# Kernel tuning notes

Hardware: AMD Instinct MI355X
Metric: run time of the kernel (lower is better)

## Reference

```python
import jax, jax.numpy as jnp
import numpy as np

B, T, M, C, H = 256, 512, 16, 16, 768  # batch, time, n_media, ctrl_dim, gru hidden


def setup_inputs() -> dict:
    key = jax.random.key(0)
    ks = jax.random.split(key, 16)
    def nrm(k, shape, s=0.05):
        return jax.random.normal(k, shape, jnp.float32) * s
    A = jnp.triu(jnp.ones((M, M), jnp.float32), 1)  # strict-upper DAG prior
    return dict(
        Xm=jax.random.uniform(ks[0], (B, T, M), jnp.float32),
        Xc=jax.random.normal(ks[1], (B, T, C), jnp.float32),
        R=jax.random.randint(ks[2], (B,), 0, 2),
        A=A,
        edge_w1=nrm(ks[3], (M, 2 * M)), edge_b1=jnp.zeros((M,), jnp.float32),
        edge_w2=nrm(ks[4], (M, M)), edge_b2=jnp.zeros((M,), jnp.float32),
        node_w=nrm(ks[5], (M, 2 * M)), node_b=jnp.zeros((M,), jnp.float32),
        W_ih=nrm(ks[6], (3 * H, M + C)), W_hh=nrm(ks[7], (3 * H, H)),
        b_ih=jnp.zeros((3 * H,), jnp.float32), b_hh=jnp.zeros((3 * H,), jnp.float32),
        wraw_w=nrm(ks[8], (M, H), 0.01), wraw_b=jnp.zeros((M,), jnp.float32),
        alpha=jnp.full((M,), 0.5, jnp.float32),
        hill_a=jax.random.uniform(ks[9], (M,), jnp.float32) * 0.8 + 0.6,
        hill_g=jax.random.uniform(ks[10], (M,), jnp.float32) * 0.3 + 0.1,
        ctrl_w=nrm(ks[11], (H, C)), ctrl_b=jnp.zeros((H,), jnp.float32),
        reg_emb=nrm(ks[12], (2, H)),
        bias=jnp.zeros((1,), jnp.float32),
        h0=jnp.zeros((1, 1, H), jnp.float32),
    )


def reference(Xm, Xc, R, A, edge_w1, edge_b1, edge_w2, edge_b2, node_w, node_b,
              W_ih, W_hh, b_ih, b_hh, wraw_w, wraw_b, alpha, hill_a, hill_g,
              ctrl_w, ctrl_b, reg_emb, bias, h0):
    Bq = Xm.shape[0]
    # --- CausalEncoder, fully batched over (B, T) ---
    send = Xm @ A.T                      # [B,T,M]
    recv = Xm @ A
    He = jax.nn.relu(jnp.concatenate([send, recv], -1) @ edge_w1.T + edge_b1)
    He = jax.nn.relu(He @ edge_w2.T + edge_b2)
    Z = jax.nn.relu(jnp.concatenate([Xm, He], -1) @ node_w.T + node_b)  # [B,T,M]
    # --- adstock: linear recurrence along time via scan ---
    a = jnp.clip(alpha, 0.0, 1.0)
    xt = jnp.swapaxes(Xm, 0, 1)          # [T,B,M]
    def ad_step(prev, x):
        cur = x + a * prev
        return cur, cur
    _, rest = jax.lax.scan(ad_step, xt[0], xt[1:])
    ads = jnp.swapaxes(jnp.concatenate([xt[:1], rest], 0), 0, 1)  # [B,T,M]
    cmax = jnp.maximum(jnp.max(ads, axis=1, keepdims=True), 1e-6)
    x_n = ads / cmax
    # --- hill saturation ---
    ha = jnp.clip(hill_a, 0.1, 3.0)
    hg = jnp.clip(hill_g, 0.1, 2.0)
    num = jnp.maximum(x_n, 0.0) ** ha
    hill = num / (num + hg ** ha + 1e-8)
    # --- GRU (PyTorch gate order r,z,n) via scan ---
    gru_in = jnp.concatenate([hill + Z, Xc], -1)       # [B,T,M+C]
    git = jnp.swapaxes(gru_in, 0, 1)                   # [T,B,M+C]
    h_init = jnp.broadcast_to(h0[0, 0], (Bq, h0.shape[-1]))
    def gru_step(h, x):
        gi = x @ W_ih.T + b_ih
        gh = h @ W_hh.T + b_hh
        ir, iz, inn = jnp.split(gi, 3, axis=-1)
        hr, hz, hn = jnp.split(gh, 3, axis=-1)
        r = jax.nn.sigmoid(ir + hr)
        z = jax.nn.sigmoid(iz + hz)
        n = jnp.tanh(inn + r * hn)
        h_new = (1.0 - z) * n + z * h
        return h_new, h_new
    _, hs = jax.lax.scan(gru_step, h_init, git)
    h_seq = jnp.swapaxes(hs, 0, 1)                     # [B,T,H]
    # --- coefficients + output heads ---
    w_pos = jax.nn.softplus(h_seq @ wraw_w.T + wraw_b)  # [B,T,M]
    w0 = 0.5 * jax.lax.stop_gradient(w_pos[:, 1]) + 0.5 * w_pos[:, 0]
    w_pos = w_pos.at[:, 0].set(w0)
    contrib = hill * w_pos
    media_term = contrib.sum(-1)                        # [B,T]
    ctrl_term = jax.nn.relu(Xc @ ctrl_w.T + ctrl_b).sum(-1) * 0.3
    reg_term = reg_emb[0].sum() * 0.3                   # original indexes with zeros
    y_scaled = media_term + ctrl_term + reg_term + bias[0]
    return y_scaled, w_pos, contrib
```

## Files before the change

### kernel.cpp

```cpp
#include <hip/hip_runtime.h>

typedef __bf16 bf16;
typedef bf16 bf16x8 __attribute__((ext_vector_type(8)));
typedef bf16 bf16x4 __attribute__((ext_vector_type(4)));
typedef float f32x4 __attribute__((ext_vector_type(4)));

#define MFMA16(a,b,c) __builtin_amdgcn_mfma_f32_16x16x32_bf16((a),(b),(c),0,0,0)

#define B_N 256
#define T_N 512
#define H_N 768
#define WROW 776
#define WIHROW 40

__device__ float    g_ctrl[B_N * T_N];
__device__ bf16     g_hbuf[2 * B_N * H_N];
__device__ unsigned g_flag[256 * 32];
__device__ unsigned g_members[8 * 32];
__device__ unsigned g_roster[8];
__device__ unsigned g_sync;

__device__ __forceinline__ float sigmoidf_(float x){ return 1.f/(1.f+__expf(-x)); }
__device__ __forceinline__ float tanhf_(float x){
  float e = __expf(-2.f*fabsf(x));
  float t = (1.f-e)/(1.f+e);
  return copysignf(t, x);
}
__device__ __forceinline__ float softplusf_(float x){
  return x > 20.f ? x : log1pf(__expf(x));
}

__global__ void k_zero() {
  const int tid = threadIdx.x;
  for (int i = tid; i < 256*32; i += 256) g_flag[i] = 0u;
  if (tid < 256) g_members[tid & 255] = 0u;
  if (tid < 8)   g_roster[tid] = 0u;
  if (tid == 0)  g_sync = 0u;
}

__global__ __launch_bounds__(256) void k_encode(
    const float* __restrict__ Xm, const float* __restrict__ Xc,
    const float* __restrict__ Aw,
    const float* __restrict__ ew1, const float* __restrict__ eb1,
    const float* __restrict__ ew2, const float* __restrict__ eb2,
    const float* __restrict__ nw,  const float* __restrict__ nb,
    const float* __restrict__ cw,  const float* __restrict__ cb,
    float* __restrict__ Zout)
{
  __shared__ float sA[16][16], sE1[16][32], sE2[16][16], sNW[16][32];
  __shared__ float sEB1[16], sEB2[16], sNB[16];
  __shared__ float sCW[768][16];
  __shared__ float sCB[768];
  const int tid = threadIdx.x;
  for (int i = tid; i < 256; i += 256) sA[i>>4][i&15] = Aw[i];
  for (int i = tid; i < 512; i += 256) sE1[i>>5][i&31] = ew1[i];
  for (int i = tid; i < 256; i += 256) sE2[i>>4][i&15] = ew2[i];
  for (int i = tid; i < 512; i += 256) sNW[i>>5][i&31] = nw[i];
  if (tid < 16) { sEB1[tid]=eb1[tid]; sEB2[tid]=eb2[tid]; sNB[tid]=nb[tid]; }
  for (int i = tid; i < 768*16; i += 256) sCW[i>>4][i&15] = cw[i];
  for (int i = tid; i < 768; i += 256) sCB[i] = cb[i];
  __syncthreads();
  const int idx = blockIdx.x*256 + tid;
  const float* xmp = Xm + (size_t)idx*16;
  const float* xcp = Xc + (size_t)idx*16;
  float xm[16], xc[16];
  #pragma unroll
  for (int j=0;j<4;j++){
    *(f32x4*)&xm[j*4] = *(const f32x4*)(xmp + j*4);
    *(f32x4*)&xc[j*4] = *(const f32x4*)(xcp + j*4);
  }
  float snd[16], rcv[16];
  #pragma unroll
  for (int i=0;i<16;i++){
    float s=0.f, r=0.f;
    #pragma unroll
    for (int j=0;j<16;j++){ s += xm[j]*sA[i][j]; r += xm[j]*sA[j][i]; }
    snd[i]=s; rcv[i]=r;
  }
  float he[16];
  #pragma unroll
  for (int i=0;i<16;i++){
    float a = sEB1[i];
    #pragma unroll
    for (int k=0;k<16;k++) a += snd[k]*sE1[i][k];
    #pragma unroll
    for (int k=0;k<16;k++) a += rcv[k]*sE1[i][16+k];
    he[i] = fmaxf(a, 0.f);
  }
  float he2[16];
  #pragma unroll
  for (int i=0;i<16;i++){
    float a = sEB2[i];
    #pragma unroll
    for (int k=0;k<16;k++) a += he[k]*sE2[i][k];
    he2[i] = fmaxf(a, 0.f);
  }
  float* zp = Zout + (size_t)idx*16;
  #pragma unroll
  for (int m=0;m<16;m++){
    float a = sNB[m];
    #pragma unroll
    for (int k=0;k<16;k++) a += xm[k]*sNW[m][k];
    #pragma unroll
    for (int k=0;k<16;k++) a += he2[k]*sNW[m][16+k];
    zp[m] = fmaxf(a, 0.f);
  }
  float cs = 0.f;
  for (int i=0;i<768;i++){
    float a = sCB[i];
    #pragma unroll
    for (int k=0;k<16;k++) a += xc[k]*sCW[i][k];
    cs += fmaxf(a, 0.f);
  }
  g_ctrl[idx] = cs * 0.3f;
}

__global__ __launch_bounds__(64) void k_adstock(
    const float* __restrict__ Xm, const float* __restrict__ alpha,
    const float* __restrict__ hill_a, const float* __restrict__ hill_g,
    float* __restrict__ Zio, float* __restrict__ hill_out)
{
  const int gid = blockIdx.x*64 + threadIdx.x;
  const int b = gid >> 4, m = gid & 15;
  float a  = fminf(fmaxf(alpha[m],  0.f),  1.f);
  float ha = fminf(fmaxf(hill_a[m], 0.1f), 3.f);
  float hg = fminf(fmaxf(hill_g[m], 0.1f), 2.f);
  float gpow = __powf(hg, ha);
  const float* xp = Xm + (size_t)b*T_N*16 + m;
  float prev = 0.f, cmax = 0.f;
  for (int t=0;t<T_N;t++){ float x = xp[(size_t)t*16]; prev = x + a*prev; cmax = fmaxf(cmax, prev); }
  cmax = fmaxf(cmax, 1e-6f);
  float inv = 1.f/cmax;
  prev = 0.f;
  float* zp  = Zio      + (size_t)b*T_N*16 + m;
  float* hp  = hill_out + (size_t)b*T_N*16 + m;
  for (int t=0;t<T_N;t++){
    float x = xp[(size_t)t*16];
    prev = x + a*prev;
    float xn  = fmaxf(prev*inv, 0.f);
    float num = __powf(xn, ha);
    float h   = num / (num + gpow + 1e-8f);
    float z   = zp[(size_t)t*16];
    hp[(size_t)t*16] = h;
    zp[(size_t)t*16] = h + z;
  }
}

__device__ __forceinline__ void poll_flags(unsigned midx, unsigned val) {
  int tries = 0;
  for (;;) {
    unsigned v = __hip_atomic_load(&g_flag[midx], __ATOMIC_RELAXED, __HIP_MEMORY_SCOPE_AGENT);
    if (__ballot(v >= val) == ~0ull) break;
    if (++tries > (1<<18)) break;
    if (tries > 8) __builtin_amdgcn_s_sleep(1);
  }
  __builtin_amdgcn_fence(__ATOMIC_ACQUIRE, "workgroup");
}

__global__ __launch_bounds__(256, 1) void k_gru(
    const float* __restrict__ Xc,
    const float* __restrict__ Wih, const float* __restrict__ Whh,
    const float* __restrict__ bih, const float* __restrict__ bhh,
    const float* __restrict__ wraww, const float* __restrict__ wrawb,
    const float* __restrict__ regemb, const float* __restrict__ bias,
    const float* __restrict__ h0,
    float* __restrict__ hillZ,
    float* __restrict__ hill,
    float* __restrict__ outy)
{
  __shared__ __align__(16) bf16 sW[88*WROW];
  __shared__ __align__(16) bf16 sWih[72*WIHROW];
  __shared__ float sGH[32][84];
  __shared__ float sGIN[32][36];
  __shared__ float sHm[32][24];
  __shared__ float sHD[32][17];
  __shared__ float sBih[72], sBhh[72];
  __shared__ float sWrb[16];
  __shared__ float sScal[2];
  __shared__ unsigned sGP[2];

  const int tid = threadIdx.x;
  const int wave = tid >> 6, lane = tid & 63;
  const int quad = lane >> 4, l16 = lane & 15;

  if (tid == 0) {
    unsigned x;
    asm volatile("s_getreg_b32 %0, hwreg(HW_REG_XCC_ID, 0, 32)" : "=s"(x));
    x &= 7u;
    unsigned slot = __hip_atomic_fetch_add(&g_roster[x], 1u,
                        __ATOMIC_RELAXED, __HIP_MEMORY_SCOPE_AGENT);
    if (slot < 32u)
      __hip_atomic_store(&g_members[x*32u + slot], (unsigned)blockIdx.x,
                         __ATOMIC_RELAXED, __HIP_MEMORY_SCOPE_AGENT);
    sGP[0] = x; sGP[1] = slot & 31u;
    __hip_atomic_fetch_add(&g_sync, 1u, __ATOMIC_RELEASE, __HIP_MEMORY_SCOPE_AGENT);
    int tries = 0;
    while (__hip_atomic_load(&g_sync, __ATOMIC_ACQUIRE, __HIP_MEMORY_SCOPE_AGENT) < 256u) {
      if (++tries > (1<<20)) break;
      __builtin_amdgcn_s_sleep(1);
    }
  }
  __syncthreads();
  const int g = (int)sGP[0], p = (int)sGP[1];
  const int j0 = p*24;
  const unsigned midx = __hip_atomic_load(&g_members[g*32 + (lane & 31)],
                            __ATOMIC_RELAXED, __HIP_MEMORY_SCOPE_AGENT) * 32u;
  const unsigned myflag = (unsigned)blockIdx.x * 32u;

  for (int c = tid; c < 88*192; c += 256) {
    int rl = c / 192, off = (c - rl*192)*4;
    const float* src = (rl < 72)
        ? &Whh[(size_t)((rl/24)*768 + j0 + (rl%24))*768 + off]
        : &wraww[(size_t)(rl-72)*768 + off];
    f32x4 w = *(const f32x4*)src;
    bf16x4 v; v[0]=(bf16)w[0]; v[1]=(bf16)w[1]; v[2]=(bf16)w[2]; v[3]=(bf16)w[3];
    *(bf16x4*)&sW[rl*WROW + off] = v;
  }
  for (int c = tid; c < 72*8; c += 256) {
    int rl = c >> 3, off = (c & 7)*4;
    int grow = (rl/24)*768 + j0 + (rl%24);
    f32x4 w = *(const f32x4*)&Wih[(size_t)grow*32 + off];
    bf16x4 v; v[0]=(bf16)w[0]; v[1]=(bf16)w[1]; v[2]=(bf16)w[2]; v[3]=(bf16)w[3];
    *(bf16x4*)&sWih[rl*WIHROW + off] = v;
  }
  if (tid < 72) {
    int grow = (tid/24)*768 + j0 + (tid%24);
    sBih[tid] = bih[grow];
    sBhh[tid] = bhh[grow];
  }
  if (tid >= 128 && tid < 144) sWrb[tid-128] = wrawb[tid-128];
  if (wave == 0) {
    float s = 0.f;
    for (int k = lane; k < 768; k += 64) s += regemb[k];
    #pragma unroll
    for (int off = 32; off; off >>= 1) s += __shfl_xor(s, off, 64);
    if (lane == 0) { sScal[0] = 0.3f*s; sScal[1] = bias[0]; }
  }
  {
    unsigned* hb = (unsigned*)g_hbuf;
    for (int e = tid; e < 384; e += 256) {
      int b = e/12, j = (e - b*12)*2;
      float f0 = h0[j0+j], f1 = h0[j0+j+1];
      sHm[b][j] = f0; sHm[b][j+1] = f1;
      union { bf16 h[2]; unsigned u; } pk;
      pk.h[0] = (bf16)f0; pk.h[1] = (bf16)f1;
      hb[((size_t)(g*32+b)*H_N + j0 + j) >> 1] = pk.u;
    }
  }
  __syncthreads();
  if (tid == 0)
    __hip_atomic_store(&g_flag[myflag], 1u, __ATOMIC_RELAXED, __HIP_MEMORY_SCOPE_AGENT);

  const int mi = wave >> 1;
  const bool lowN = !(wave & 1);
  const int batch_l = l16 + mi*16;
  const int gb = g*32 + batch_l;
  const int bq = g*32 + p;
  const float regt = sScal[0], bias0 = sScal[1];
  const int r0 = lowN ? l16        : 48 + l16;
  const int r1 = lowN ? 16 + l16   : min(64 + l16, 71);
  const int rX = lowN ? 32 + l16   : 72 + l16;
  const int rh = 72 + l16;

  bf16x8 bw0[24], bw1[24];
  #pragma unroll
  for (int kt = 0; kt < 24; kt++) {
    const int ko = kt*32 + quad*8;
    bw0[kt] = *(const bf16x8*)&sW[r0*WROW + ko];
    bw1[kt] = *(const bf16x8*)&sW[r1*WROW + ko];
  }
  const bf16x8 wf0 = *(const bf16x8*)&sWih[r0*WIHROW + quad*8];
  const bf16x8 wf1 = *(const bf16x8*)&sWih[r1*WIHROW + quad*8];
  const bf16x8 wf2 = lowN ? *(const bf16x8*)&sWih[(32+l16)*WIHROW + quad*8] : wf0;

  float wp0_r = 0.f, hl0_r = 0.f, ct0_r = 0.f;

  f32x4 xf0, xf1;
  {
    const float* hz = hillZ + (size_t)gb*T_N*16;
    const float* xr = Xc    + (size_t)gb*T_N*16;
    const float* src = (quad < 2) ? (hz + quad*8) : (xr + (quad-2)*8);
    xf0 = *(const f32x4*)src;
    xf1 = *(const f32x4*)(src + 4);
  }
  float hl_pf = 0.f, ct_pf = 0.f;
  if (tid < 16) {
    hl_pf = hill[(size_t)bq*T_N*16 + tid];
    if (tid == 0) ct_pf = g_ctrl[(size_t)bq*T_N];
  }

  const bf16* hb_base = g_hbuf;
  int par = 0;
  for (int t = 0; t < T_N; t++) {
    f32x4 a0 = {0.f,0.f,0.f,0.f}, a1 = a0, a2 = a0, gi0 = a0, gi1 = a0, hd = a0;
    {
      bf16x8 ax;
      ax[0]=(bf16)xf0[0]; ax[1]=(bf16)xf0[1]; ax[2]=(bf16)xf0[2]; ax[3]=(bf16)xf0[3];
      ax[4]=(bf16)xf1[0]; ax[5]=(bf16)xf1[1]; ax[6]=(bf16)xf1[2]; ax[7]=(bf16)xf1[3];
      if (lowN) {
        a0 = MFMA16(ax, wf0, a0);
        a1 = MFMA16(ax, wf1, a1);
        a2 = MFMA16(ax, wf2, a2);
      } else {
        gi0 = MFMA16(ax, wf0, gi0);
        gi1 = MFMA16(ax, wf1, gi1);
      }
    }
    poll_flags(midx, (unsigned)(t + 1));
    bf16x8 hf[24];
    {
      const bf16* hrow = hb_base + (size_t)par*B_N*H_N + (size_t)gb*H_N + quad*8;
      #pragma unroll
      for (int kt = 0; kt < 24; kt++) {
        asm volatile("global_load_dwordx4 %0, %1, off sc0"
                     : "=v"(hf[kt]) : "v"(hrow + kt*32) : "memory");
      }
      asm volatile("s_waitcnt vmcnt(0)"
          : "+v"(hf[0]),"+v"(hf[1]),"+v"(hf[2]),"+v"(hf[3]),
            "+v"(hf[4]),"+v"(hf[5]),"+v"(hf[6]),"+v"(hf[7]) :: "memory");
      asm volatile(""
          : "+v"(hf[8]),"+v"(hf[9]),"+v"(hf[10]),"+v"(hf[11]),
            "+v"(hf[12]),"+v"(hf[13]),"+v"(hf[14]),"+v"(hf[15]));
      asm volatile(""
          : "+v"(hf[16]),"+v"(hf[17]),"+v"(hf[18]),"+v"(hf[19]),
            "+v"(hf[20]),"+v"(hf[21]),"+v"(hf[22]),"+v"(hf[23]));
    }
    {
      const int tn = (t + 1 < T_N) ? t + 1 : T_N - 1;
      const float* hz = hillZ + ((size_t)gb*T_N + tn)*16;
      const float* xr = Xc    + ((size_t)gb*T_N + tn)*16;
      const float* src = (quad < 2) ? (hz + quad*8) : (xr + (quad-2)*8);
      xf0 = *(const f32x4*)src;
      xf1 = *(const f32x4*)(src + 4);
    }
    #pragma unroll
    for (int kt = 0; kt < 24; kt++) {
      const int ko = kt*32 + quad*8;
      a0 = MFMA16(hf[kt], bw0[kt], a0);
      a1 = MFMA16(hf[kt], bw1[kt], a1);
      if (lowN) a2 = MFMA16(hf[kt], *(const bf16x8*)&sW[rX*WROW + ko], a2);
      else      hd = MFMA16(hf[kt], *(const bf16x8*)&sW[rX*WROW + ko], hd);
    }
    {
      const int rb = mi*16 + quad*4;
      const int c0 = lowN ? l16 : 48 + l16;
      const int c1 = lowN ? 16 + l16 : 64 + l16;
      #pragma unroll
      for (int r = 0; r < 4; r++) {
        sGH[rb + r][c0] = a0[r];
        sGH[rb + r][c1] = a1[r];
        if (lowN) sGH[rb + r][32 + l16] = a2[r];
        else { sGIN[rb + r][l16] = gi0[r]; sGIN[rb + r][16 + l16] = gi1[r];
               sHD[rb + r][l16] = hd[r]; }
      }
    }
    __syncthreads();
    float hd_s = 0.f;
    if (tid < 16) hd_s = sHD[p][tid];
    if (tid >= 32) {
      unsigned* hnxt = (unsigned*)(g_hbuf + (size_t)(1-par)*B_N*H_N);
      for (int e = tid - 32; e < 384; e += 224) {
        int b = e/12, j = (e - b*12)*2;
        float hn0, hn1;
        {
          float rr = sigmoidf_(sGH[b][j]    + sBih[j]    + sBhh[j]);
          float zz = sigmoidf_(sGH[b][24+j] + sBih[24+j] + sBhh[24+j]);
          float hh = sGH[b][48+j] + sBhh[48+j];
          float in_ = sGIN[b][j]  + sBih[48+j];
          float nn = tanhf_(in_ + rr*hh);
          hn0 = (1.f-zz)*nn + zz*sHm[b][j];
        }
        {
          int j1 = j+1;
          float rr = sigmoidf_(sGH[b][j1]    + sBih[j1]    + sBhh[j1]);
          float zz = sigmoidf_(sGH[b][24+j1] + sBih[24+j1] + sBhh[24+j1]);
          float hh = sGH[b][48+j1] + sBhh[48+j1];
          float in_ = sGIN[b][j1]  + sBih[48+j1];
          float nn = tanhf_(in_ + rr*hh);
          hn1 = (1.f-zz)*nn + zz*sHm[b][j1];
        }
        sHm[b][j] = hn0; sHm[b][j+1] = hn1;
        union { bf16 h[2]; unsigned u; } pk;
        pk.h[0] = (bf16)hn0; pk.h[1] = (bf16)hn1;
        hnxt[((size_t)(g*32+b)*H_N + j0 + j) >> 1] = pk.u;
      }
    }
    __syncthreads();
    if (tid == 0)
      __hip_atomic_store(&g_flag[myflag], (unsigned)(t + 2), __ATOMIC_RELAXED, __HIP_MEMORY_SCOPE_AGENT);
    if (t > 0 && tid < 16) {
      const int tt = t - 1;
      float wp = softplusf_(hd_s + sWrb[tid]);
      float hl = hl_pf;
      if (tt == 0) { wp0_r = wp; hl0_r = hl; ct0_r = ct_pf; }
      else {
        size_t o = (size_t)bq*T_N + tt;
        float cv = hl*wp;
        hillZ[o*16 + tid] = wp;
        hill[o*16 + tid]  = cv;
        float cs = cv;
        cs += __shfl_xor(cs, 8, 64);
        cs += __shfl_xor(cs, 4, 64);
        cs += __shfl_xor(cs, 2, 64);
        cs += __shfl_xor(cs, 1, 64);
        if (tid == 0) outy[o] = cs + ct_pf + regt + bias0;
        if (tt == 1) {
          float w0 = 0.5f*(wp + wp0_r);
          float c0v = hl0_r*w0;
          size_t o0 = (size_t)bq*T_N;
          hillZ[o0*16 + tid] = w0;
          hill[o0*16 + tid]  = c0v;
          float cs0 = c0v;
          cs0 += __shfl_xor(cs0, 8, 64);
          cs0 += __shfl_xor(cs0, 4, 64);
          cs0 += __shfl_xor(cs0, 2, 64);
          cs0 += __shfl_xor(cs0, 1, 64);
          if (tid == 0) outy[o0] = cs0 + ct0_r + regt + bias0;
        }
      }
    }
    if (tid < 16) {
      hl_pf = hill[((size_t)bq*T_N + t)*16 + tid];
      if (tid == 0) ct_pf = g_ctrl[(size_t)bq*T_N + t];
    }
    par ^= 1;
  }
  if (wave & 1) {
    poll_flags(midx, (unsigned)(T_N + 1));
    const bf16* hrow = hb_base + (size_t)par*B_N*H_N + (size_t)gb*H_N + quad*8;
    f32x4 hd = {0.f,0.f,0.f,0.f};
    bf16x8 hf[24];
    #pragma unroll
    for (int kt = 0; kt < 24; kt++) {
      asm volatile("global_load_dwordx4 %0, %1, off sc0"
                   : "=v"(hf[kt]) : "v"(hrow + kt*32) : "memory");
    }
    asm volatile("s_waitcnt vmcnt(0)"
        : "+v"(hf[0]),"+v"(hf[1]),"+v"(hf[2]),"+v"(hf[3]),
          "+v"(hf[4]),"+v"(hf[5]),"+v"(hf[6]),"+v"(hf[7]) :: "memory");
    asm volatile(""
        : "+v"(hf[8]),"+v"(hf[9]),"+v"(hf[10]),"+v"(hf[11]),
          "+v"(hf[12]),"+v"(hf[13]),"+v"(hf[14]),"+v"(hf[15]));
    asm volatile(""
        : "+v"(hf[16]),"+v"(hf[17]),"+v"(hf[18]),"+v"(hf[19]),
          "+v"(hf[20]),"+v"(hf[21]),"+v"(hf[22]),"+v"(hf[23]));
    #pragma unroll
    for (int kt = 0; kt < 24; kt++) {
      const int ko = kt*32 + quad*8;
      hd = MFMA16(hf[kt], *(const bf16x8*)&sW[rh*WROW + ko], hd);
    }
    const int rb = mi*16 + quad*4;
    #pragma unroll
    for (int r = 0; r < 4; r++) sHD[rb + r][l16] = hd[r];
  }
  __syncthreads();
  if (tid < 16) {
    const int tt = T_N - 1;
    float wp = softplusf_(sHD[p][tid] + sWrb[tid]);
    float hl = hill[((size_t)bq*T_N + tt)*16 + tid];
    size_t o = (size_t)bq*T_N + tt;
    float cv = hl*wp;
    hillZ[o*16 + tid] = wp;
    hill[o*16 + tid]  = cv;
    float cs = cv;
    cs += __shfl_xor(cs, 8, 64);
    cs += __shfl_xor(cs, 4, 64);
    cs += __shfl_xor(cs, 2, 64);
    cs += __shfl_xor(cs, 1, 64);
    if (tid == 0) outy[o] = cs + g_ctrl[o] + regt + bias0;
  }
}

extern "C" void kernel_launch(void* const* d_in, const int* in_sizes, int n_in,
                              void* d_out, int out_size, void* d_ws, size_t ws_size,
                              hipStream_t stream) {
  const float* Xm    = (const float*)d_in[0];
  const float* Xc    = (const float*)d_in[1];
  const float* Aw    = (const float*)d_in[3];
  const float* ew1   = (const float*)d_in[4];
  const float* eb1   = (const float*)d_in[5];
  const float* ew2   = (const float*)d_in[6];
  const float* eb2   = (const float*)d_in[7];
  const float* nw    = (const float*)d_in[8];
  const float* nb    = (const float*)d_in[9];
  const float* Wih   = (const float*)d_in[10];
  const float* Whh   = (const float*)d_in[11];
  const float* bih   = (const float*)d_in[12];
  const float* bhh   = (const float*)d_in[13];
  const float* wraww = (const float*)d_in[14];
  const float* wrawb = (const float*)d_in[15];
  const float* alpha = (const float*)d_in[16];
  const float* hilla = (const float*)d_in[17];
  const float* hillg = (const float*)d_in[18];
  const float* cw    = (const float*)d_in[19];
  const float* cb    = (const float*)d_in[20];
  const float* regemb= (const float*)d_in[21];
  const float* bias  = (const float*)d_in[22];
  const float* h0    = (const float*)d_in[23];

  float* outy = (float*)d_out;
  float* outw = outy + 256*512;
  float* outc = outw + 256*512*16;

  k_zero<<<1, 256, 0, stream>>>();
  k_encode<<<512, 256, 0, stream>>>(Xm, Xc, Aw, ew1, eb1, ew2, eb2, nw, nb, cw, cb,
                                    outw);
  k_adstock<<<64, 64, 0, stream>>>(Xm, alpha, hilla, hillg, outw, outc);
  k_gru<<<dim3(256), dim3(256), 0, stream>>>(
      Xc, Wih, Whh, bih, bhh, wraww, wrawb, regemb, bias, h0,
      outw, outc, outy);
}
```

Measured before the change: 3.584 ms.

## Split GRU step into two 16-batch halves with split-K waves and LDS-staged h

Result: faster. 2.941 ms (-17.9%).

```diff
diff --git a/kernel.cpp b/kernel.cpp
--- a/kernel.cpp
+++ b/kernel.cpp
@@ -11,11 +11,10 @@
 #define T_N 512
 #define H_N 768
 #define WROW 776
-#define WIHROW 40
 
 __device__ float    g_ctrl[B_N * T_N];
 __device__ bf16     g_hbuf[2 * B_N * H_N];
-__device__ unsigned g_flag[256 * 32];
+__device__ unsigned g_flag[256 * 64];
 __device__ unsigned g_members[8 * 32];
 __device__ unsigned g_roster[8];
 __device__ unsigned g_sync;
@@ -29,11 +28,19 @@
 __device__ __forceinline__ float softplusf_(float x){
   return x > 20.f ? x : log1pf(__expf(x));
 }
+__device__ __forceinline__ bf16x8 ld_bf8(const float* p){
+  f32x4 a = *(const f32x4*)p;
+  f32x4 b = *(const f32x4*)(p + 4);
+  bf16x8 v;
+  v[0]=(bf16)a[0]; v[1]=(bf16)a[1]; v[2]=(bf16)a[2]; v[3]=(bf16)a[3];
+  v[4]=(bf16)b[0]; v[5]=(bf16)b[1]; v[6]=(bf16)b[2]; v[7]=(bf16)b[3];
+  return v;
+}
 
 __global__ void k_zero() {
   const int tid = threadIdx.x;
-  for (int i = tid; i < 256*32; i += 256) g_flag[i] = 0u;
-  if (tid < 256) g_members[tid & 255] = 0u;
+  for (int i = tid; i < 256*64; i += 256) g_flag[i] = 0u;
+  if (tid < 256) g_members[tid] = 0u;
   if (tid < 8)   g_roster[tid] = 0u;
   if (tid == 0)  g_sync = 0u;
 }
@@ -168,12 +175,11 @@
     float* __restrict__ hill,
     float* __restrict__ outy)
 {
-  __shared__ __align__(16) bf16 sW[88*WROW];
-  __shared__ __align__(16) bf16 sWih[72*WIHROW];
-  __shared__ float sGH[32][84];
-  __shared__ float sGIN[32][36];
-  __shared__ float sHm[32][24];
-  __shared__ float sHD[32][17];
+  __shared__ __align__(16) bf16 sW2[32*WROW];
+  __shared__ __align__(16) bf16 sH[16*768];
+  __shared__ float sGH2[2][16][100];
+  __shared__ float sGIN[16][32];
+  __shared__ float sHm[32][26];
   __shared__ float sBih[72], sBhh[72];
   __shared__ float sWrb[16];
   __shared__ float sScal[2];
@@ -182,6 +188,8 @@
   const int tid = threadIdx.x;
   const int wave = tid >> 6, lane = tid & 63;
   const int quad = lane >> 4, l16 = lane & 15;
+  const int rg = wave & 1;
+  const int kh = wave >> 1;
 
   if (tid == 0) {
     unsigned x;
@@ -203,25 +211,23 @@
   __syncthreads();
   const int g = (int)sGP[0], p = (int)sGP[1];
   const int j0 = p*24;
-  const unsigned midx = __hip_atomic_load(&g_members[g*32 + (lane & 31)],
-                            __ATOMIC_RELAXED, __HIP_MEMORY_SCOPE_AGENT) * 32u;
-  const unsigned myflag = (unsigned)blockIdx.x * 32u;
-
-  for (int c = tid; c < 88*192; c += 256) {
+  const int s_own = (p >= 16) ? 1 : 0;
+  const int bqL = p & 15;
+  const int bq = g*32 + p;
+  const unsigned member = __hip_atomic_load(&g_members[g*32 + (lane & 31)],
+                              __ATOMIC_RELAXED, __HIP_MEMORY_SCOPE_AGENT);
+  const unsigned midx0 = member * 64u;
+  const unsigned myflag = (unsigned)blockIdx.x * 64u;
+
+  for (int c = tid; c < 32*192; c += 256) {
     int rl = c / 192, off = (c - rl*192)*4;
-    const float* src = (rl < 72)
-        ? &Whh[(size_t)((rl/24)*768 + j0 + (rl%24))*768 + off]
-        : &wraww[(size_t)(rl-72)*768 + off];
-    f32x4 w = *(const f32x4*)src;
+    int L = (rl < 16) ? (32 + rl) : (64 + rl);
+    f32x4 w;
+    if (L < 72)      w = *(const f32x4*)&Whh[(size_t)((L/24)*768 + j0 + (L%24))*768 + off];
+    else if (L < 88) w = *(const f32x4*)&wraww[(size_t)(L-72)*768 + off];
+    else             { w[0]=0.f; w[1]=0.f; w[2]=0.f; w[3]=0.f; }
     bf16x4 v; v[0]=(bf16)w[0]; v[1]=(bf16)w[1]; v[2]=(bf16)w[2]; v[3]=(bf16)w[3];
-    *(bf16x4*)&sW[rl*WROW + off] = v;
-  }
-  for (int c = tid; c < 72*8; c += 256) {
-    int rl = c >> 3, off = (c & 7)*4;
-    int grow = (rl/24)*768 + j0 + (rl%24);
-    f32x4 w = *(const f32x4*)&Wih[(size_t)grow*32 + off];
-    bf16x4 v; v[0]=(bf16)w[0]; v[1]=(bf16)w[1]; v[2]=(bf16)w[2]; v[3]=(bf16)w[3];
-    *(bf16x4*)&sWih[rl*WIHROW + off] = v;
+    *(bf16x4*)&sW2[rl*WROW + off] = v;
   }
   if (tid < 72) {
     int grow = (tid/24)*768 + j0 + (tid%24);
@@ -230,12 +236,48 @@
   }
   if (tid >= 128 && tid < 144) sWrb[tid-128] = wrawb[tid-128];
   if (wave == 0) {
-    float s = 0.f;
-    for (int k = lane; k < 768; k += 64) s += regemb[k];
-    #pragma unroll
-    for (int off = 32; off; off >>= 1) s += __shfl_xor(s, off, 64);
-    if (lane == 0) { sScal[0] = 0.3f*s; sScal[1] = bias[0]; }
-  }
+    float sacc = 0.f;
+    for (int k = lane; k < 768; k += 64) sacc += regemb[k];
+    #pragma unroll
+    for (int off = 32; off; off >>= 1) sacc += __shfl_xor(sacc, off, 64);
+    if (lane == 0) { sScal[0] = 0.3f*sacc; sScal[1] = bias[0]; }
+  }
+
+  bf16x8 bw0[12], bw1[12];
+  {
+    const int LA = (rg ? 48 : 0) + l16;
+    const int LB = (rg ? 64 : 16) + l16;
+    const float* rowA = Whh + (size_t)((LA/24)*768 + j0 + (LA%24))*768;
+    const float* rowB = (LB < 72)
+        ? (Whh + (size_t)((LB/24)*768 + j0 + (LB%24))*768)
+        : (wraww + (size_t)(LB-72)*768);
+    #pragma unroll
+    for (int kk = 0; kk < 12; kk++) {
+      const int col = (kh*12 + kk)*32 + quad*8;
+      bw0[kk] = ld_bf8(rowA + col);
+      bw1[kk] = ld_bf8(rowB + col);
+    }
+  }
+  bf16x8 wf0, wf1, wf2;
+  #pragma unroll
+  for (int i = 0; i < 8; i++) { wf0[i]=(bf16)0.f; wf1[i]=(bf16)0.f; wf2[i]=(bf16)0.f; }
+  if (kh == 0) {
+    const int base = rg ? 48 : 0;
+    {
+      const int L = base + l16;
+      wf0 = ld_bf8(Wih + (size_t)((L/24)*768 + j0 + (L%24))*32 + quad*8);
+    }
+    {
+      const int L = base + 16 + l16;
+      if (L < 72)
+        wf1 = ld_bf8(Wih + (size_t)((L/24)*768 + j0 + (L%24))*32 + quad*8);
+    }
+    if (rg == 0) {
+      const int L = 32 + l16;
+      wf2 = ld_bf8(Wih + (size_t)((L/24)*768 + j0 + (L%24))*32 + quad*8);
+    }
+  }
+
   {
     unsigned* hb = (unsigned*)g_hbuf;
     for (int e = tid; e < 384; e += 256) {
@@ -248,37 +290,20 @@
     }
   }
   __syncthreads();
-  if (tid == 0)
-    __hip_atomic_store(&g_flag[myflag], 1u, __ATOMIC_RELAXED, __HIP_MEMORY_SCOPE_AGENT);
-
-  const int mi = wave >> 1;
-  const bool lowN = !(wave & 1);
-  const int batch_l = l16 + mi*16;
-  const int gb = g*32 + batch_l;
-  const int bq = g*32 + p;
+  if (tid == 0) {
+    __hip_atomic_store(&g_flag[myflag],      1u, __ATOMIC_RELAXED, __HIP_MEMORY_SCOPE_AGENT);
+    __hip_atomic_store(&g_flag[myflag + 32], 1u, __ATOMIC_RELAXED, __HIP_MEMORY_SCOPE_AGENT);
+  }
   const float regt = sScal[0], bias0 = sScal[1];
-  const int r0 = lowN ? l16        : 48 + l16;
-  const int r1 = lowN ? 16 + l16   : min(64 + l16, 71);
-  const int rX = lowN ? 32 + l16   : 72 + l16;
-  const int rh = 72 + l16;
-
-  bf16x8 bw0[24], bw1[24];
-  #pragma unroll
-  for (int kt = 0; kt < 24; kt++) {
-    const int ko = kt*32 + quad*8;
-    bw0[kt] = *(const bf16x8*)&sW[r0*WROW + ko];
-    bw1[kt] = *(const bf16x8*)&sW[r1*WROW + ko];
-  }
-  const bf16x8 wf0 = *(const bf16x8*)&sWih[r0*WIHROW + quad*8];
-  const bf16x8 wf1 = *(const bf16x8*)&sWih[r1*WIHROW + quad*8];
-  const bf16x8 wf2 = lowN ? *(const bf16x8*)&sWih[(32+l16)*WIHROW + quad*8] : wf0;
 
   float wp0_r = 0.f, hl0_r = 0.f, ct0_r = 0.f;
 
   f32x4 xf0, xf1;
-  {
-    const float* hz = hillZ + (size_t)gb*T_N*16;
-    const float* xr = Xc    + (size_t)gb*T_N*16;
+  xf0[0]=0.f; xf0[1]=0.f; xf0[2]=0.f; xf0[3]=0.f; xf1 = xf0;
+  if (kh == 0) {
+    const int gb0 = g*32 + l16;
+    const float* hz = hillZ + (size_t)gb0*T_N*16;
+    const float* xr = Xc    + (size_t)gb0*T_N*16;
     const float* src = (quad < 2) ? (hz + quad*8) : (xr + (quad-2)*8);
     xf0 = *(const f32x4*)src;
     xf1 = *(const f32x4*)(src + 4);
@@ -290,184 +315,230 @@
   }
 
   const bf16* hb_base = g_hbuf;
+  const int rl3 = (rg ? 16 : 0) + l16;
+  const int swz = (l16 & 7) << 3;
   int par = 0;
+
+  #pragma unroll 1
   for (int t = 0; t < T_N; t++) {
-    f32x4 a0 = {0.f,0.f,0.f,0.f}, a1 = a0, a2 = a0, gi0 = a0, gi1 = a0, hd = a0;
+    #pragma unroll 1
+    for (int s = 0; s < 2; s++) {
+      poll_flags(midx0 + (unsigned)(s*32), (unsigned)(t + 1));
+      {
+        const int gbv = g*32 + s*16 + l16;
+        const bf16* hsrc = hb_base + (size_t)par*B_N*H_N + (size_t)gbv*H_N + quad*8;
+        bf16x8 hv[6];
+        #pragma unroll
+        for (int j = 0; j < 6; j++) {
+          asm volatile("global_load_dwordx4 %0, %1, off sc0"
+                       : "=v"(hv[j]) : "v"(hsrc + (wave*6 + j)*32) : "memory");
+        }
+        asm volatile("s_waitcnt vmcnt(0)"
+            : "+v"(hv[0]),"+v"(hv[1]),"+v"(hv[2]),"+v"(hv[3]),"+v"(hv[4]),"+v"(hv[5])
+            :: "memory");
+        bf16* dst = &sH[l16*768];
+        #pragma unroll
+        for (int j = 0; j < 6; j++) {
+          const int cv = wave*6 + j;
+          *(bf16x8*)&dst[(cv*32 + quad*8) ^ swz] = hv[j];
+        }
+      }
+      bf16x8 ax;
+      if (kh == 0) {
+        ax[0]=(bf16)xf0[0]; ax[1]=(bf16)xf0[1]; ax[2]=(bf16)xf0[2]; ax[3]=(bf16)xf0[3];
+        ax[4]=(bf16)xf1[0]; ax[5]=(bf16)xf1[1]; ax[6]=(bf16)xf1[2]; ax[7]=(bf16)xf1[3];
+      }
+      __syncthreads();
+      f32x4 a0; a0[0]=0.f; a0[1]=0.f; a0[2]=0.f; a0[3]=0.f;
+      f32x4 a1 = a0, a2 = a0, gi0 = a0, gi1 = a0;
+      if (kh == 0) {
+        if (rg == 0) {
+          a0 = MFMA16(ax, wf0, a0);
+          a1 = MFMA16(ax, wf1, a1);
+          a2 = MFMA16(ax, wf2, a2);
+        } else {
+          gi0 = MFMA16(ax, wf0, gi0);
+          gi1 = MFMA16(ax, wf1, gi1);
+        }
+      }
+      if (kh == 0) {
+        const int sn = s ^ 1;
+        int tn = (s == 1) ? t + 1 : t;
+        if (tn >= T_N) tn = T_N - 1;
+        const int gbn = g*32 + sn*16 + l16;
+        const float* hz = hillZ + ((size_t)gbn*T_N + tn)*16;
+        const float* xr = Xc    + ((size_t)gbn*T_N + tn)*16;
+        const float* src = (quad < 2) ? (hz + quad*8) : (xr + (quad-2)*8);
+        xf0 = *(const f32x4*)src;
+        xf1 = *(const f32x4*)(src + 4);
+      }
+      {
+        const bf16* hrow = &sH[l16*768];
+        #pragma unroll
+        for (int kk = 0; kk < 12; kk++) {
+          const int kt = kh*12 + kk;
+          bf16x8 ha = *(const bf16x8*)&hrow[(kt*32 + quad*8) ^ swz];
+          a0 = MFMA16(ha, bw0[kk], a0);
+          a1 = MFMA16(ha, bw1[kk], a1);
+          a2 = MFMA16(ha, *(const bf16x8*)&sW2[rl3*WROW + kt*32 + quad*8], a2);
+        }
+      }
+      {
+        const int c0 = rg*48 + l16;
+        #pragma unroll
+        for (int r = 0; r < 4; r++) {
+          const int rb = quad*4 + r;
+          sGH2[kh][rb][c0]    = a0[r];
+          sGH2[kh][rb][c0+16] = a1[r];
+          sGH2[kh][rb][c0+32] = a2[r];
+        }
+        if (kh == 0 && rg == 1) {
+          #pragma unroll
+          for (int r = 0; r < 4; r++) {
+            const int rb = quad*4 + r;
+            sGIN[rb][l16]    = gi0[r];
+            sGIN[rb][16+l16] = gi1[r];
+          }
+        }
+      }
+      __syncthreads();
+      const bool own = (s_own == s);
+      float hd_s = 0.f;
+      if (own && tid < 16) hd_s = sGH2[0][bqL][72+tid] + sGH2[1][bqL][72+tid];
+      if (tid >= 64) {
+        const int e = tid - 64;
+        const int b = e / 12, jp = (e - b*12)*2;
+        const int bg = s*16 + b;
+        unsigned* hnxt = (unsigned*)(g_hbuf + (size_t)(1-par)*B_N*H_N);
+        float hn0, hn1;
+        {
+          const int j = jp;
+          float gh_r = sGH2[0][b][j]    + sGH2[1][b][j];
+          float gh_z = sGH2[0][b][24+j] + sGH2[1][b][24+j];
+          float gh_n = sGH2[0][b][48+j] + sGH2[1][b][48+j];
+          float rr = sigmoidf_(gh_r + sBih[j]    + sBhh[j]);
+          float zz = sigmoidf_(gh_z + sBih[24+j] + sBhh[24+j]);
+          float nn = tanhf_(sGIN[b][j] + sBih[48+j] + rr*(gh_n + sBhh[48+j]));
+          hn0 = (1.f-zz)*nn + zz*sHm[bg][j];
+        }
+        {
+          const int j = jp + 1;
+          float gh_r = sGH2[0][b][j]    + sGH2[1][b][j];
+          float gh_z = sGH2[0][b][24+j] + sGH2[1][b][24+j];
+          float gh_n = sGH2[0][b][48+j] + sGH2[1][b][48+j];
+          float rr = sigmoidf_(gh_r + sBih[j]    + sBhh[j]);
+          float zz = sigmoidf_(gh_z + sBih[24+j] + sBhh[24+j]);
+          float nn = tanhf_(sGIN[b][j] + sBih[48+j] + rr*(gh_n + sBhh[48+j]));
+          hn1 = (1.f-zz)*nn + zz*sHm[bg][j];
+        }
+        sHm[bg][jp] = hn0; sHm[bg][jp+1] = hn1;
+        union { bf16 h[2]; unsigned u; } pk;
+        pk.h[0] = (bf16)hn0; pk.h[1] = (bf16)hn1;
+        hnxt[((size_t)(g*32+bg)*H_N + j0 + jp) >> 1] = pk.u;
+      }
+      __syncthreads();
+      if (tid == 0)
+        __hip_atomic_store(&g_flag[myflag + s*32], (unsigned)(t + 2),
+                           __ATOMIC_RELAXED, __HIP_MEMORY_SCOPE_AGENT);
+      if (own) {
+        if (t > 0 && tid < 16) {
+          const int tt = t - 1;
+          float wp = softplusf_(hd_s + sWrb[tid]);
+          float hl = hl_pf;
+          if (tt == 0) { wp0_r = wp; hl0_r = hl; ct0_r = ct_pf; }
+          else {
+            size_t o = (size_t)bq*T_N + tt;
+            float cv = hl*wp;
+            hillZ[o*16 + tid] = wp;
+            hill[o*16 + tid]  = cv;
+            float cs = cv;
+            cs += __shfl_xor(cs, 8, 64);
+            cs += __shfl_xor(cs, 4, 64);
+            cs += __shfl_xor(cs, 2, 64);
+            cs += __shfl_xor(cs, 1, 64);
+            if (tid == 0) outy[o] = cs + ct_pf + regt + bias0;
+            if (tt == 1) {
+              float w0 = 0.5f*(wp + wp0_r);
+              float c0v = hl0_r*w0;
+              size_t o0 = (size_t)bq*T_N;
+              hillZ[o0*16 + tid] = w0;
+              hill[o0*16 + tid]  = c0v;
+              float cs0 = c0v;
+              cs0 += __shfl_xor(cs0, 8, 64);
+              cs0 += __shfl_xor(cs0, 4, 64);
+              cs0 += __shfl_xor(cs0, 2, 64);
+              cs0 += __shfl_xor(cs0, 1, 64);
+              if (tid == 0) outy[o0] = cs0 + ct0_r + regt + bias0;
+            }
+          }
+        }
+        if (tid < 16) {
+          hl_pf = hill[((size_t)bq*T_N + t)*16 + tid];
+          if (tid == 0) ct_pf = g_ctrl[(size_t)bq*T_N + t];
+        }
+      }
+    }
+    par ^= 1;
+  }
+
+  {
+    const int s = s_own;
+    poll_flags(midx0 + (unsigned)(s*32), (unsigned)(T_N + 1));
     {
-      bf16x8 ax;
-      ax[0]=(bf16)xf0[0]; ax[1]=(bf16)xf0[1]; ax[2]=(bf16)xf0[2]; ax[3]=(bf16)xf0[3];
-      ax[4]=(bf16)xf1[0]; ax[5]=(bf16)xf1[1]; ax[6]=(bf16)xf1[2]; ax[7]=(bf16)xf1[3];
-      if (lowN) {
-        a0 = MFMA16(ax, wf0, a0);
-        a1 = MFMA16(ax, wf1, a1);
-        a2 = MFMA16(ax, wf2, a2);
-      } else {
-        gi0 = MFMA16(ax, wf0, gi0);
-        gi1 = MFMA16(ax, wf1, gi1);
-      }
-    }
-    poll_flags(midx, (unsigned)(t + 1));
-    bf16x8 hf[24];
-    {
-      const bf16* hrow = hb_base + (size_t)par*B_N*H_N + (size_t)gb*H_N + quad*8;
+      const int gbv = g*32 + s*16 + l16;
+      const bf16* hsrc = hb_base + (size_t)par*B_N*H_N + (size_t)gbv*H_N + quad*8;
+      bf16x8 hv[6];
       #pragma unroll
-      for (int kt = 0; kt < 24; kt++) {
+      for (int j = 0; j < 6; j++) {
         asm volatile("global_load_dwordx4 %0, %1, off sc0"
-                     : "=v"(hf[kt]) : "v"(hrow + kt*32) : "memory");
+                     : "=v"(hv[j]) : "v"(hsrc + (wave*6 + j)*32) : "memory");
       }
       asm volatile("s_waitcnt vmcnt(0)"
-          : "+v"(hf[0]),"+v"(hf[1]),"+v"(hf[2]),"+v"(hf[3]),
-            "+v"(hf[4]),"+v"(hf[5]),"+v"(hf[6]),"+v"(hf[7]) :: "memory");
-      asm volatile(""
-          : "+v"(hf[8]),"+v"(hf[9]),"+v"(hf[10]),"+v"(hf[11]),
-            "+v"(hf[12]),"+v"(hf[13]),"+v"(hf[14]),"+v"(hf[15]));
-      asm volatile(""
-          : "+v"(hf[16]),"+v"(hf[17]),"+v"(hf[18]),"+v"(hf[19]),
-            "+v"(hf[20]),"+v"(hf[21]),"+v"(hf[22]),"+v"(hf[23]));
-    }
-    {
-      const int tn = (t + 1 < T_N) ? t + 1 : T_N - 1;
-      const float* hz = hillZ + ((size_t)gb*T_N + tn)*16;
-      const float* xr = Xc    + ((size_t)gb*T_N + tn)*16;
-      const float* src = (quad < 2) ? (hz + quad*8) : (xr + (quad-2)*8);
-      xf0 = *(const f32x4*)src;
-      xf1 = *(const f32x4*)(src + 4);
-    }
-    #pragma unroll
-    for (int kt = 0; kt < 24; kt++) {
-      const int ko = kt*32 + quad*8;
-      a0 = MFMA16(hf[kt], bw0[kt], a0);
-      a1 = MFMA16(hf[kt], bw1[kt], a1);
-      if (lowN) a2 = MFMA16(hf[kt], *(const bf16x8*)&sW[rX*WROW + ko], a2);
-      else      hd = MFMA16(hf[kt], *(const bf16x8*)&sW[rX*WROW + ko], hd);
-    }
-    {
-      const int rb = mi*16 + quad*4;
-      const int c0 = lowN ? l16 : 48 + l16;
-      const int c1 = lowN ? 16 + l16 : 64 + l16;
+          : "+v"(hv[0]),"+v"(hv[1]),"+v"(hv[2]),"+v"(hv[3]),"+v"(hv[4]),"+v"(hv[5])
+          :: "memory");
+      bf16* dst = &sH[l16*768];
+      #pragma unroll
+      for (int j = 0; j < 6; j++) {
+        const int cv = wave*6 + j;
+        *(bf16x8*)&dst[(cv*32 + quad*8) ^ swz] = hv[j];
+      }
+    }
+    __syncthreads();
+    if (rg == 1) {
+      f32x4 a1; a1[0]=0.f; a1[1]=0.f; a1[2]=0.f; a1[3]=0.f;
+      f32x4 a2 = a1;
+      const bf16* hrow = &sH[l16*768];
+      #pragma unroll
+      for (int kk = 0; kk < 12; kk++) {
+        const int kt = kh*12 + kk;
+        bf16x8 ha = *(const bf16x8*)&hrow[(kt*32 + quad*8) ^ swz];
+        a1 = MFMA16(ha, bw1[kk], a1);
+        a2 = MFMA16(ha, *(const bf16x8*)&sW2[(16+l16)*WROW + kt*32 + quad*8], a2);
+      }
       #pragma unroll
       for (int r = 0; r < 4; r++) {
-        sGH[rb + r][c0] = a0[r];
-        sGH[rb + r][c1] = a1[r];
-        if (lowN) sGH[rb + r][32 + l16] = a2[r];
-        else { sGIN[rb + r][l16] = gi0[r]; sGIN[rb + r][16 + l16] = gi1[r];
-               sHD[rb + r][l16] = hd[r]; }
+        const int rb = quad*4 + r;
+        sGH2[kh][rb][64 + l16] = a1[r];
+        sGH2[kh][rb][80 + l16] = a2[r];
       }
     }
     __syncthreads();
-    float hd_s = 0.f;
-    if (tid < 16) hd_s = sHD[p][tid];
-    if (tid >= 32) {
-      unsigned* hnxt = (unsigned*)(g_hbuf + (size_t)(1-par)*B_N*H_N);
-      for (int e = tid - 32; e < 384; e += 224) {
-        int b = e/12, j = (e - b*12)*2;
-        float hn0, hn1;
-        {
-          float rr = sigmoidf_(sGH[b][j]    + sBih[j]    + sBhh[j]);
-          float zz = sigmoidf_(sGH[b][24+j] + sBih[24+j] + sBhh[24+j]);
-          float hh = sGH[b][48+j] + sBhh[48+j];
-          float in_ = sGIN[b][j]  + sBih[48+j];
-          float nn = tanhf_(in_ + rr*hh);
-          hn0 = (1.f-zz)*nn + zz*sHm[b][j];
-        }
-        {
-          int j1 = j+1;
-          float rr = sigmoidf_(sGH[b][j1]    + sBih[j1]    + sBhh[j1]);
-          float zz = sigmoidf_(sGH[b][24+j1] + sBih[24+j1] + sBhh[24+j1]);
-          float hh = sGH[b][48+j1] + sBhh[48+j1];
-          float in_ = sGIN[b][j1]  + sBih[48+j1];
-          float nn = tanhf_(in_ + rr*hh);
-          hn1 = (1.f-zz)*nn + zz*sHm[b][j1];
-        }
-        sHm[b][j] = hn0; sHm[b][j+1] = hn1;
-        union { bf16 h[2]; unsigned u; } pk;
-        pk.h[0] = (bf16)hn0; pk.h[1] = (bf16)hn1;
-        hnxt[((size_t)(g*32+b)*H_N + j0 + j) >> 1] = pk.u;
-      }
-    }
-    __syncthreads();
-    if (tid == 0)
-      __hip_atomic_store(&g_flag[myflag], (unsigned)(t + 2), __ATOMIC_RELAXED, __HIP_MEMORY_SCOPE_AGENT);
-    if (t > 0 && tid < 16) {
-      const int tt = t - 1;
-      float wp = softplusf_(hd_s + sWrb[tid]);
-      float hl = hl_pf;
-      if (tt == 0) { wp0_r = wp; hl0_r = hl; ct0_r = ct_pf; }
-      else {
-        size_t o = (size_t)bq*T_N + tt;
-        float cv = hl*wp;
-        hillZ[o*16 + tid] = wp;
-        hill[o*16 + tid]  = cv;
-        float cs = cv;
-        cs += __shfl_xor(cs, 8, 64);
-        cs += __shfl_xor(cs, 4, 64);
-        cs += __shfl_xor(cs, 2, 64);
-        cs += __shfl_xor(cs, 1, 64);
-        if (tid == 0) outy[o] = cs + ct_pf + regt + bias0;
-        if (tt == 1) {
-          float w0 = 0.5f*(wp + wp0_r);
-          float c0v = hl0_r*w0;
-          size_t o0 = (size_t)bq*T_N;
-          hillZ[o0*16 + tid] = w0;
-          hill[o0*16 + tid]  = c0v;
-          float cs0 = c0v;
-          cs0 += __shfl_xor(cs0, 8, 64);
-          cs0 += __shfl_xor(cs0, 4, 64);
-          cs0 += __shfl_xor(cs0, 2, 64);
-          cs0 += __shfl_xor(cs0, 1, 64);
-          if (tid == 0) outy[o0] = cs0 + ct0_r + regt + bias0;
-        }
-      }
-    }
     if (tid < 16) {
-      hl_pf = hill[((size_t)bq*T_N + t)*16 + tid];
-      if (tid == 0) ct_pf = g_ctrl[(size_t)bq*T_N + t];
-    }
-    par ^= 1;
-  }
-  if (wave & 1) {
-    poll_flags(midx, (unsigned)(T_N + 1));
-    const bf16* hrow = hb_base + (size_t)par*B_N*H_N + (size_t)gb*H_N + quad*8;
-    f32x4 hd = {0.f,0.f,0.f,0.f};
-    bf16x8 hf[24];
-    #pragma unroll
-    for (int kt = 0; kt < 24; kt++) {
-      asm volatile("global_load_dwordx4 %0, %1, off sc0"
-                   : "=v"(hf[kt]) : "v"(hrow + kt*32) : "memory");
-    }
-    asm volatile("s_waitcnt vmcnt(0)"
-        : "+v"(hf[0]),"+v"(hf[1]),"+v"(hf[2]),"+v"(hf[3]),
-          "+v"(hf[4]),"+v"(hf[5]),"+v"(hf[6]),"+v"(hf[7]) :: "memory");
-    asm volatile(""
-        : "+v"(hf[8]),"+v"(hf[9]),"+v"(hf[10]),"+v"(hf[11]),
-          "+v"(hf[12]),"+v"(hf[13]),"+v"(hf[14]),"+v"(hf[15]));
-    asm volatile(""
-        : "+v"(hf[16]),"+v"(hf[17]),"+v"(hf[18]),"+v"(hf[19]),
-          "+v"(hf[20]),"+v"(hf[21]),"+v"(hf[22]),"+v"(hf[23]));
-    #pragma unroll
-    for (int kt = 0; kt < 24; kt++) {
-      const int ko = kt*32 + quad*8;
-      hd = MFMA16(hf[kt], *(const bf16x8*)&sW[rh*WROW + ko], hd);
-    }
-    const int rb = mi*16 + quad*4;
-    #pragma unroll
-    for (int r = 0; r < 4; r++) sHD[rb + r][l16] = hd[r];
-  }
-  __syncthreads();
-  if (tid < 16) {
-    const int tt = T_N - 1;
-    float wp = softplusf_(sHD[p][tid] + sWrb[tid]);
-    float hl = hill[((size_t)bq*T_N + tt)*16 + tid];
-    size_t o = (size_t)bq*T_N + tt;
-    float cv = hl*wp;
-    hillZ[o*16 + tid] = wp;
-    hill[o*16 + tid]  = cv;
-    float cs = cv;
-    cs += __shfl_xor(cs, 8, 64);
-    cs += __shfl_xor(cs, 4, 64);
-    cs += __shfl_xor(cs, 2, 64);
-    cs += __shfl_xor(cs, 1, 64);
-    if (tid == 0) outy[o] = cs + g_ctrl[o] + regt + bias0;
+      const int tt = T_N - 1;
+      float hd = sGH2[0][bqL][72+tid] + sGH2[1][bqL][72+tid];
+      float wp = softplusf_(hd + sWrb[tid]);
+      float hl = hill[((size_t)bq*T_N + tt)*16 + tid];
+      size_t o = (size_t)bq*T_N + tt;
+      float cv = hl*wp;
+      hillZ[o*16 + tid] = wp;
+      hill[o*16 + tid]  = cv;
+      float cs = cv;
+      cs += __shfl_xor(cs, 8, 64);
+      cs += __shfl_xor(cs, 4, 64);
+      cs += __shfl_xor(cs, 2, 64);
+      cs += __shfl_xor(cs, 1, 64);
+      if (tid == 0) outy[o] = cs + g_ctrl[o] + regt + bias0;
+    }
   }
 }
 
```
